# Optimization experiments

Measured on AMD Instinct MI355X. Metric: run time of the kernel, lower is better.

Reference implementation:

```python
import jax, jax.numpy as jnp
import numpy as np

KS, ST, SS, TOP_N, WIN = 32, 16, 64, 16, 512  # kernel_size, stride, select_size, top_n, window_size
NEG = -1e30


def setup_inputs() -> dict:
    key = jax.random.key(0)
    k0, k1, k2, k3 = jax.random.split(key, 4)
    B, S, H, Dqk, Dv = 1, 2048, 16, 128, 128
    q = jax.random.normal(k0, (B, S, H, Dqk), jnp.float32)
    k = jax.random.normal(k1, (B, S, H, Dqk), jnp.float32)
    v = jax.random.normal(k2, (B, S, H, Dv), jnp.float32)
    w_gate = jax.random.normal(k3, (Dqk, 3), jnp.float32) * (Dqk ** -0.5)
    b_gate = jnp.zeros((3,), jnp.float32)
    return {"q": q, "k": k, "v": v, "w_gate": w_gate, "b_gate": b_gate}


def _masked_probs(scores, mask):
    # numerically safe masked softmax; rows with no valid key yield all-zero probs
    s = jnp.where(mask, scores, NEG)
    lse = jax.nn.logsumexp(s, axis=-1, keepdims=True)
    return jnp.where(mask, jnp.exp(s - lse), 0.0)


def _nsa_forward(q, k, v, w_gate, b_gate):
    B, S, H, Dqk = q.shape
    scale = Dqk ** -0.5
    C = (S - KS) // ST + 1          # number of compressed blocks
    NSEL = S // SS                  # number of selection blocks
    tpos = jnp.arange(S)

    # ---- branch 1: compressed attention (mean-pooled K/V blocks) ----
    wpos = jnp.arange(C)[:, None] * ST + jnp.arange(KS)[None, :]   # [C,KS]
    cmp_k = k[:, wpos].mean(axis=2)                                # [B,C,H,Dqk]
    cmp_v = v[:, wpos].mean(axis=2)                                # [B,C,H,Dv]
    s_cmp = jnp.einsum('bqhd,bchd->bhqc', q, cmp_k) * scale
    cmp_end = jnp.arange(C) * ST + KS - 1
    cmask = cmp_end[None, :] <= tpos[:, None]                      # block fully in past
    p_cmp = _masked_probs(s_cmp, cmask)                            # [B,H,S,C]
    cmp_o = jnp.einsum('bhqc,bchd->bqhd', p_cmp, cmp_v)

    # ---- top-n block selection from compressed attention probs ----
    c_start = jnp.arange(C) * ST
    j_start = jnp.arange(NSEL) * SS
    overlap = ((c_start[:, None] < j_start[None, :] + SS) &
               (c_start[:, None] + KS > j_start[None, :])).astype(q.dtype)  # [C,NSEL]
    p_sel = jnp.einsum('bhqc,cj->bhqj', p_cmp, overlap)            # [B,H,S,NSEL]
    allowed = j_start[None, :] <= tpos[:, None]                    # block started
    cur_oh = jax.nn.one_hot(tpos // SS, NSEL, dtype=q.dtype)       # force current block
    sc = jnp.where(allowed, p_sel, -1.0) + 1e6 * cur_oh
    _, idx = jax.lax.top_k(sc, TOP_N)                              # [B,H,S,TOP_N]

    # ---- shared dense scores (reference only; real kernel is IO-aware) ----
    s_full = jnp.einsum('bqhd,bkhd->bhqk', q, k) * scale           # [B,H,S,S]
    causal = tpos[None, :] <= tpos[:, None]

    # ---- branch 2: selected-block attention ----
    blk_mask = (idx[..., None] == jnp.arange(NSEL)).any(axis=-2)   # [B,H,S,NSEL]
    key_blk = tpos // SS
    sel_mask = blk_mask[..., key_blk] & causal                     # [B,H,S,S]
    p_s = _masked_probs(s_full, sel_mask)
    select_o = jnp.einsum('bhqk,bkhd->bqhd', p_s, v)

    # ---- branch 3: sliding-window causal attention ----
    wmask = causal & ((tpos[:, None] - tpos[None, :]) <= WIN)
    p_w = _masked_probs(s_full, wmask)
    window_o = jnp.einsum('bhqk,bkhd->bqhd', p_w, v)

    # ---- learned per-query gates ----
    gate = jax.nn.sigmoid(jnp.einsum('bqhd,dg->bqhg', q, w_gate) + b_gate)
    return (cmp_o * gate[..., 0:1] + select_o * gate[..., 1:2]
            + window_o * gate[..., 2:3])


def reference(q, k, v, w_gate, b_gate):
    return _nsa_forward(q, k, v, w_gate, b_gate)
```

## Files before the change

### kernel.cpp

```cpp
#include <hip/hip_runtime.h>

#define S_LEN 2048
#define NH 16
#define DIM 128
#define KSZ 32
#define STRD 16
#define SSZ 64
#define NSELB 32
#define NCMP 127
#define TOPN 16
#define WINSZ 512
#define NEGF (-1e30f)
#define NEGTH (-1e29f)
#define SCALE 0.088388347648318447f

typedef __attribute__((ext_vector_type(8))) short bf16x8;
typedef __attribute__((ext_vector_type(4))) float f32x4;

__device__ __forceinline__ unsigned short f2bf(float f) {
  unsigned u = __builtin_bit_cast(unsigned, f);
  return (unsigned short)((u + 0x7FFFu + ((u >> 16) & 1u)) >> 16);
}
__device__ __forceinline__ bf16x8 pack8(const float* f) {
  bf16x8 r;
#pragma unroll
  for (int i = 0; i < 8; ++i) r[i] = (short)f2bf(f[i]);
  return r;
}

__global__ __launch_bounds__(256) void vt_build(const float* __restrict__ v,
                                                unsigned short* __restrict__ vtg) {
  const int c = blockIdx.x * 256 + threadIdx.x;
  const int h = c >> 15;
  const int rem = c & 32767;
  const int d = rem >> 8;
  const int tc = rem & 255;
  float f[8];
#pragma unroll
  for (int i = 0; i < 8; ++i) f[i] = v[((tc * 8 + i) * NH + h) * DIM + d];
  bf16x8 r = pack8(f);
  *(bf16x8*)(vtg + ((h * DIM + d) * S_LEN + tc * 8)) = r;
}

__global__ __launch_bounds__(128) void nsa_compress(
    const float* __restrict__ k, const float* __restrict__ v,
    unsigned short* __restrict__ cmpkb, unsigned short* __restrict__ cmpvt) {
  const int c = blockIdx.x & 127;
  const int h = blockIdx.x >> 7;
  const int d = threadIdx.x;
  float sk = 0.f, sv = 0.f;
  if (c < NCMP) {
    const int base = ((c * STRD) * NH + h) * DIM + d;
#pragma unroll
    for (int i = 0; i < KSZ; ++i) {
      sk += k[base + i * NH * DIM];
      sv += v[base + i * NH * DIM];
    }
    sk *= (1.0f / KSZ); sv *= (1.0f / KSZ);
  }
  cmpkb[(h * 128 + c) * 128 + d] = (c < NCMP) ? f2bf(sk) : 0;
  cmpvt[(h * 128 + d) * 128 + c] = (c < NCMP) ? f2bf(sv) : 0;
}

__global__ __launch_bounds__(256, 2) void nsa_main(
    const float* __restrict__ q, const float* __restrict__ k,
    const float* __restrict__ v, const float* __restrict__ wg,
    const float* __restrict__ bg, const unsigned short* __restrict__ vtg,
    const unsigned short* __restrict__ cmpkb, const unsigned short* __restrict__ cmpvt,
    float* __restrict__ out) {
  __shared__ __align__(16) char klds[32 * 256];
  __shared__ __align__(16) char vt[128 * 80];
  __shared__ __align__(16) float sc[4 * 16 * 132];
  __shared__ __align__(16) char pa[4 * 2048];
  __shared__ unsigned maskLds[64];
  __shared__ unsigned unionLds;
  __shared__ float gatesLds[192];

  const int h = blockIdx.x >> 5;
  const int t0 = (blockIdx.x & 31) * 64;
  const int tid = threadIdx.x;
  const int lane = tid & 63;
  const int w = tid >> 6;
  const int l15 = lane & 15;
  const int l4 = lane >> 4;

  float* scw = sc + w * 16 * 132;
  char* paw = pa + w * 2048;

  if (tid < 64) maskLds[tid] = 0u;
  if (tid == 64) unionLds = 0u;

  {
    const int qloc = tid >> 2, g = tid & 3;
    if (g < 3) {
      const int tq = t0 + qloc;
      const float* qr = q + (tq * NH + h) * DIM;
      float acc = bg[g];
#pragma unroll
      for (int d4 = 0; d4 < DIM; d4 += 4) {
        const float4 qv = *(const float4*)(qr + d4);
        acc += qv.x * wg[(d4 + 0) * 3 + g] + qv.y * wg[(d4 + 1) * 3 + g] +
               qv.z * wg[(d4 + 2) * 3 + g] + qv.w * wg[(d4 + 3) * 3 + g];
      }
      gatesLds[qloc * 3 + g] = 1.0f / (1.0f + __expf(-acc));
    }
  }

  bf16x8 qf[4];
  {
    const float* qp = q + ((t0 + w * 16 + l15) * NH + h) * DIM + l4 * 8;
#pragma unroll
    for (int ks = 0; ks < 4; ++ks) {
      float f[8];
#pragma unroll
      for (int i = 0; i < 4; ++i) f[i] = qp[ks * 32 + i];
#pragma unroll
      for (int i = 0; i < 4; ++i) f[4 + i] = qp[ks * 32 + 4 + i];
      qf[ks] = pack8(f);
    }
  }

  for (int ct = 0; ct < 4; ++ct) {
    __syncthreads();
#pragma unroll
    for (int c = 0; c < 2; ++c) {
      const int e = tid + c * 256;
      const int key = e >> 4, dc = e & 15;
      *(bf16x8*)(klds + key * 256 + ((dc * 16) ^ ((key & 7) << 4))) =
          *(const bf16x8*)(cmpkb + (h * 128 + ct * 32 + key) * 128 + dc * 8);
    }
    __syncthreads();
    f32x4 s0 = {0, 0, 0, 0}, s1 = {0, 0, 0, 0};
#pragma unroll
    for (int ks = 0; ks < 4; ++ks) {
      const int db = ks * 64 + l4 * 16;
      bf16x8 b0 = *(const bf16x8*)(klds + l15 * 256 + (db ^ ((l15 & 7) << 4)));
      bf16x8 b1 = *(const bf16x8*)(klds + (16 + l15) * 256 + (db ^ (((16 + l15) & 7) << 4)));
      s0 = __builtin_amdgcn_mfma_f32_16x16x32_bf16(qf[ks], b0, s0, 0, 0, 0);
      s1 = __builtin_amdgcn_mfma_f32_16x16x32_bf16(qf[ks], b1, s1, 0, 0, 0);
    }
#pragma unroll
    for (int j = 0; j < 4; ++j) {
      const int qr = l4 * 4 + j;
      scw[qr * 132 + ct * 32 + l15] = s0[j] * SCALE;
      scw[qr * 132 + ct * 32 + 16 + l15] = s1[j] * SCALE;
    }
  }
  __syncthreads();

  {
    const int qq = lane >> 2, qg = lane & 3;
    const int tq = t0 + w * 16 + qq;
    const int nv = (tq >= KSZ - 1) ? ((tq - (KSZ - 1)) / STRD + 1) : 0;
    float x[32];
#pragma unroll
    for (int i = 0; i < 32; ++i) x[i] = scw[qq * 132 + qg * 32 + i];
    float m = NEGF;
#pragma unroll
    for (int i = 0; i < 32; ++i) {
      const int c = qg * 32 + i;
      if (c < nv) m = fmaxf(m, x[i]);
    }
    m = fmaxf(m, __shfl_xor(m, 1));
    m = fmaxf(m, __shfl_xor(m, 2));
    float s = 0.f;
#pragma unroll
    for (int i = 0; i < 32; ++i) {
      const int c = qg * 32 + i;
      x[i] = (c < nv) ? __expf(x[i] - m) : 0.f;
      s += x[i];
    }
    s += __shfl_xor(s, 1);
    s += __shfl_xor(s, 2);
    const float inv = (nv > 0) ? (1.0f / s) : 0.f;
#pragma unroll
    for (int i = 0; i < 32; ++i) scw[qq * 132 + qg * 32 + i] = x[i] * inv;
  }
  __syncthreads();

  {
    const int qq = lane >> 2, jg = lane & 3;
    const int tq = t0 + w * 16 + qq;
    float* ss = (float*)paw;
    float vj[8];
#pragma unroll
    for (int i = 0; i < 8; ++i) {
      const int j = jg * 8 + i;
      const int lo = (4 * j - 1 > 0) ? 4 * j - 1 : 0;
      const int hi = (4 * j + 3 < NCMP - 1) ? 4 * j + 3 : NCMP - 1;
      float ps = 0.f;
      for (int c = lo; c <= hi; ++c) ps += scw[qq * 132 + c];
      float val = (j * SSZ <= tq) ? ps : -1.0f;
      if (j == (tq >> 6)) val += 1e6f;
      vj[i] = val;
      ss[qq * 32 + j] = val;
    }
    __syncthreads();
#pragma unroll
    for (int i = 0; i < 8; ++i) {
      const int j = jg * 8 + i;
      const float my = vj[i];
      int rank = 0;
      for (int jp = 0; jp < NSELB; ++jp) {
        const float o = ss[qq * 32 + jp];
        rank += (o > my) || (o == my && jp < j);
      }
      if (rank < TOPN && (j * SSZ <= tq)) {
        atomicOr(&maskLds[w * 16 + qq], 1u << j);
        atomicOr(&unionLds, 1u << j);
      }
    }
  }
  __syncthreads();

  unsigned maskq[4];
#pragma unroll
  for (int j = 0; j < 4; ++j) maskq[j] = maskLds[w * 16 + l4 * 4 + j];
  const unsigned unionMask = unionLds;

  f32x4 accA[8], accB[8];
#pragma unroll
  for (int n = 0; n < 8; ++n) accA[n] = (f32x4){0, 0, 0, 0};
  for (int ct = 0; ct < 4; ++ct) {
    __syncthreads();
#pragma unroll
    for (int c = 0; c < 2; ++c) {
      const int e = tid + c * 256;
      const int d = e >> 2, kc = e & 3;
      *(bf16x8*)(vt + d * 80 + kc * 16) =
          *(const bf16x8*)(cmpvt + (h * 128 + d) * 128 + ct * 32 + kc * 8);
    }
    __syncthreads();
    float f[8];
#pragma unroll
    for (int i = 0; i < 8; ++i) f[i] = scw[l15 * 132 + ct * 32 + l4 * 8 + i];
    bf16x8 ap = pack8(f);
#pragma unroll
    for (int n = 0; n < 8; ++n) {
      bf16x8 bv = *(const bf16x8*)(vt + (n * 16 + l15) * 80 + l4 * 16);
      accA[n] = __builtin_amdgcn_mfma_f32_16x16x32_bf16(ap, bv, accA[n], 0, 0, 0);
    }
  }
  __syncthreads();
#pragma unroll
  for (int j = 0; j < 4; ++j) {
    const int qr = l4 * 4 + j;
    const float g0 = gatesLds[(w * 16 + qr) * 3 + 0];
#pragma unroll
    for (int n = 0; n < 8; ++n) scw[qr * 132 + n * 16 + l15] = g0 * accA[n][j];
  }

  float mS[4], lS[4], mW[4], lW[4];
#pragma unroll
  for (int j = 0; j < 4; ++j) { mS[j] = NEGF; lS[j] = 0.f; mW[j] = NEGF; lW[j] = 0.f; }
#pragma unroll
  for (int n = 0; n < 8; ++n) { accA[n] = (f32x4){0, 0, 0, 0}; accB[n] = (f32x4){0, 0, 0, 0}; }

  const int ktmax = (t0 + 63) >> 5;
  for (int kt = 0; kt <= ktmax; ++kt) {
    const int kt0 = kt * 32;
    const int jb = kt >> 1;
    const bool selAny = (unionMask >> jb) & 1u;
    const bool winAny = (kt0 + 31) >= (t0 - WINSZ);
    if (!selAny && !winAny) continue;
    __syncthreads();
#pragma unroll
    for (int c = 0; c < 2; ++c) {
      const int e = tid + c * 256;
      const int key = e >> 4, dc = e & 15;
      const float* src = k + ((kt0 + key) * NH + h) * DIM + dc * 8;
      float f[8];
#pragma unroll
      for (int i = 0; i < 8; ++i) f[i] = src[i];
      *(bf16x8*)(klds + key * 256 + ((dc * 16) ^ ((key & 7) << 4))) = pack8(f);
    }
#pragma unroll
    for (int c = 0; c < 2; ++c) {
      const int e = tid + c * 256;
      const int d = e >> 2, kc = e & 3;
      *(bf16x8*)(vt + d * 80 + kc * 16) =
          *(const bf16x8*)(vtg + (h * 128 + d) * S_LEN + kt0 + kc * 8);
    }
    __syncthreads();

    f32x4 s0 = {0, 0, 0, 0}, s1 = {0, 0, 0, 0};
#pragma unroll
    for (int ks = 0; ks < 4; ++ks) {
      const int db = ks * 64 + l4 * 16;
      bf16x8 b0 = *(const bf16x8*)(klds + l15 * 256 + (db ^ ((l15 & 7) << 4)));
      bf16x8 b1 = *(const bf16x8*)(klds + (16 + l15) * 256 + (db ^ (((16 + l15) & 7) << 4)));
      s0 = __builtin_amdgcn_mfma_f32_16x16x32_bf16(qf[ks], b0, s0, 0, 0, 0);
      s1 = __builtin_amdgcn_mfma_f32_16x16x32_bf16(qf[ks], b1, s1, 0, 0, 0);
    }
#pragma unroll
    for (int j = 0; j < 4; ++j) { s0[j] *= SCALE; s1[j] *= SCALE; }
    const int c0 = kt0 + l15, c1 = kt0 + 16 + l15;

    if (selAny) {
#pragma unroll
      for (int j = 0; j < 4; ++j) {
        const int qr = l4 * 4 + j;
        const int tq = t0 + w * 16 + qr;
        const bool mb = (maskq[j] >> jb) & 1u;
        const float v0 = (mb && c0 <= tq) ? s0[j] : NEGF;
        const float v1 = (mb && c1 <= tq) ? s1[j] : NEGF;
        float rm = fmaxf(v0, v1);
        rm = fmaxf(rm, __shfl_xor(rm, 1));
        rm = fmaxf(rm, __shfl_xor(rm, 2));
        rm = fmaxf(rm, __shfl_xor(rm, 4));
        rm = fmaxf(rm, __shfl_xor(rm, 8));
        const float mn = fmaxf(mS[j], rm);
        const float sf = __expf(mS[j] - mn);
        const float p0 = (v0 > NEGTH) ? __expf(v0 - mn) : 0.f;
        const float p1 = (v1 > NEGTH) ? __expf(v1 - mn) : 0.f;
        float rs = p0 + p1;
        rs += __shfl_xor(rs, 1);
        rs += __shfl_xor(rs, 2);
        rs += __shfl_xor(rs, 4);
        rs += __shfl_xor(rs, 8);
        lS[j] = lS[j] * sf + rs;
        mS[j] = mn;
#pragma unroll
        for (int n = 0; n < 8; ++n) accA[n][j] *= sf;
        *(unsigned short*)(paw + qr * 128 + ((l15 * 2) ^ ((qr & 7) << 4))) = f2bf(p0);
        *(unsigned short*)(paw + qr * 128 + (((16 + l15) * 2) ^ ((qr & 7) << 4))) = f2bf(p1);
      }
      bf16x8 ap = *(const bf16x8*)(paw + l15 * 128 + ((l4 * 16) ^ ((l15 & 7) << 4)));
#pragma unroll
      for (int n = 0; n < 8; ++n) {
        bf16x8 bv = *(const bf16x8*)(vt + (n * 16 + l15) * 80 + l4 * 16);
        accA[n] = __builtin_amdgcn_mfma_f32_16x16x32_bf16(ap, bv, accA[n], 0, 0, 0);
      }
    }
    if (winAny) {
#pragma unroll
      for (int j = 0; j < 4; ++j) {
        const int qr = l4 * 4 + j;
        const int tq = t0 + w * 16 + qr;
        const float v0 = (c0 <= tq && c0 >= tq - WINSZ) ? s0[j] : NEGF;
        const float v1 = (c1 <= tq && c1 >= tq - WINSZ) ? s1[j] : NEGF;
        float rm = fmaxf(v0, v1);
        rm = fmaxf(rm, __shfl_xor(rm, 1));
        rm = fmaxf(rm, __shfl_xor(rm, 2));
        rm = fmaxf(rm, __shfl_xor(rm, 4));
        rm = fmaxf(rm, __shfl_xor(rm, 8));
        const float mn = fmaxf(mW[j], rm);
        const float sf = __expf(mW[j] - mn);
        const float p0 = (v0 > NEGTH) ? __expf(v0 - mn) : 0.f;
        const float p1 = (v1 > NEGTH) ? __expf(v1 - mn) : 0.f;
        float rs = p0 + p1;
        rs += __shfl_xor(rs, 1);
        rs += __shfl_xor(rs, 2);
        rs += __shfl_xor(rs, 4);
        rs += __shfl_xor(rs, 8);
        lW[j] = lW[j] * sf + rs;
        mW[j] = mn;
#pragma unroll
        for (int n = 0; n < 8; ++n) accB[n][j] *= sf;
        *(unsigned short*)(paw + qr * 128 + ((l15 * 2) ^ ((qr & 7) << 4))) = f2bf(p0);
        *(unsigned short*)(paw + qr * 128 + (((16 + l15) * 2) ^ ((qr & 7) << 4))) = f2bf(p1);
      }
      bf16x8 ap = *(const bf16x8*)(paw + l15 * 128 + ((l4 * 16) ^ ((l15 & 7) << 4)));
#pragma unroll
      for (int n = 0; n < 8; ++n) {
        bf16x8 bv = *(const bf16x8*)(vt + (n * 16 + l15) * 80 + l4 * 16);
        accB[n] = __builtin_amdgcn_mfma_f32_16x16x32_bf16(ap, bv, accB[n], 0, 0, 0);
      }
    }
  }

#pragma unroll
  for (int j = 0; j < 4; ++j) {
    const int qr = l4 * 4 + j;
    const int tq = t0 + w * 16 + qr;
    const float g1 = gatesLds[(w * 16 + qr) * 3 + 1];
    const float g2 = gatesLds[(w * 16 + qr) * 3 + 2];
    const float rlS = 1.0f / lS[j];
    const float rlW = 1.0f / lW[j];
#pragma unroll
    for (int n = 0; n < 8; ++n) {
      const float val = scw[qr * 132 + n * 16 + l15] + g1 * accA[n][j] * rlS +
                        g2 * accB[n][j] * rlW;
      out[(tq * NH + h) * DIM + n * 16 + l15] = val;
    }
  }
}

extern "C" void kernel_launch(void* const* d_in, const int* in_sizes, int n_in,
                              void* d_out, int out_size, void* d_ws, size_t ws_size,
                              hipStream_t stream) {
  const float* q  = (const float*)d_in[0];
  const float* k  = (const float*)d_in[1];
  const float* v  = (const float*)d_in[2];
  const float* wg = (const float*)d_in[3];
  const float* bg = (const float*)d_in[4];
  float* out = (float*)d_out;

  unsigned short* vtg   = (unsigned short*)d_ws;
  unsigned short* cmpkb = vtg + NH * DIM * S_LEN;
  unsigned short* cmpvt = cmpkb + NH * 128 * 128;

  vt_build<<<2048, 256, 0, stream>>>(v, vtg);
  nsa_compress<<<NH * 128, 128, 0, stream>>>(k, v, cmpkb, cmpvt);
  nsa_main<<<NH * 32, 256, 0, stream>>>(q, k, v, wg, bg, vtg, cmpkb, cmpvt, out);
}
```

Measured before the change: 242.0 us.

## Split compressed QK into bf16 hi/lo terms and pre-convert K to bf16

Computes the compressed-attention scores with a three-term bf16 split (hi*hi + lo*hi + hi*lo), so top-k block selection is closer to fp32 precision. K is converted to bf16 once in a pre-pass, which removes the per-block fp32 load and convert inside the main loop. The online softmax now rescales only when the running max rises. The gated compressed output is kept in registers instead of LDS, which drops one barrier. The split adds MFMA work and LDS loads in the compressed stage, plus extra registers and workspace.

```diff
diff --git a/kernel.cpp b/kernel.cpp
--- a/kernel.cpp
+++ b/kernel.cpp
@@ -21,6 +21,9 @@
   unsigned u = __builtin_bit_cast(unsigned, f);
   return (unsigned short)((u + 0x7FFFu + ((u >> 16) & 1u)) >> 16);
 }
+__device__ __forceinline__ float bf2f(unsigned short b) {
+  return __builtin_bit_cast(float, (unsigned)b << 16);
+}
 __device__ __forceinline__ bf16x8 pack8(const float* f) {
   bf16x8 r;
 #pragma unroll
@@ -28,23 +31,32 @@
   return r;
 }
 
-__global__ __launch_bounds__(256) void vt_build(const float* __restrict__ v,
-                                                unsigned short* __restrict__ vtg) {
+__global__ __launch_bounds__(256) void nsa_build(
+    const float* __restrict__ v, const float* __restrict__ k,
+    unsigned short* __restrict__ vtg, unsigned short* __restrict__ kb) {
   const int c = blockIdx.x * 256 + threadIdx.x;
-  const int h = c >> 15;
-  const int rem = c & 32767;
-  const int d = rem >> 8;
-  const int tc = rem & 255;
-  float f[8];
-#pragma unroll
-  for (int i = 0; i < 8; ++i) f[i] = v[((tc * 8 + i) * NH + h) * DIM + d];
-  bf16x8 r = pack8(f);
-  *(bf16x8*)(vtg + ((h * DIM + d) * S_LEN + tc * 8)) = r;
+  {
+    const int h = c >> 15, rem = c & 32767;
+    const int d = rem >> 8, tc = rem & 255;
+    float f[8];
+#pragma unroll
+    for (int i = 0; i < 8; ++i) f[i] = v[((tc * 8 + i) * NH + h) * DIM + d];
+    *(bf16x8*)(vtg + ((h * DIM + d) * S_LEN + tc * 8)) = pack8(f);
+  }
+  {
+    const int t = c >> 8, h2 = (c >> 4) & 15, dc = c & 15;
+    const float* src = k + ((t * NH + h2) * DIM + dc * 8);
+    float f[8];
+#pragma unroll
+    for (int i = 0; i < 8; ++i) f[i] = src[i];
+    *(bf16x8*)(kb + (t * NH + h2) * DIM + dc * 8) = pack8(f);
+  }
 }
 
 __global__ __launch_bounds__(128) void nsa_compress(
     const float* __restrict__ k, const float* __restrict__ v,
-    unsigned short* __restrict__ cmpkb, unsigned short* __restrict__ cmpvt) {
+    unsigned short* __restrict__ cmpkh, unsigned short* __restrict__ cmpkl,
+    unsigned short* __restrict__ cmpvt) {
   const int c = blockIdx.x & 127;
   const int h = blockIdx.x >> 7;
   const int d = threadIdx.x;
@@ -58,16 +70,19 @@
     }
     sk *= (1.0f / KSZ); sv *= (1.0f / KSZ);
   }
-  cmpkb[(h * 128 + c) * 128 + d] = (c < NCMP) ? f2bf(sk) : 0;
+  const unsigned short hi = f2bf(sk);
+  const unsigned short lo = f2bf(sk - bf2f(hi));
+  cmpkh[(h * 128 + c) * 128 + d] = (c < NCMP) ? hi : 0;
+  cmpkl[(h * 128 + c) * 128 + d] = (c < NCMP) ? lo : 0;
   cmpvt[(h * 128 + d) * 128 + c] = (c < NCMP) ? f2bf(sv) : 0;
 }
 
 __global__ __launch_bounds__(256, 2) void nsa_main(
-    const float* __restrict__ q, const float* __restrict__ k,
-    const float* __restrict__ v, const float* __restrict__ wg,
-    const float* __restrict__ bg, const unsigned short* __restrict__ vtg,
-    const unsigned short* __restrict__ cmpkb, const unsigned short* __restrict__ cmpvt,
-    float* __restrict__ out) {
+    const float* __restrict__ q, const float* __restrict__ wg,
+    const float* __restrict__ bg, const unsigned short* __restrict__ kb,
+    const unsigned short* __restrict__ vtg,
+    const unsigned short* __restrict__ cmpkh, const unsigned short* __restrict__ cmpkl,
+    const unsigned short* __restrict__ cmpvt, float* __restrict__ out) {
   __shared__ __align__(16) char klds[32 * 256];
   __shared__ __align__(16) char vt[128 * 80];
   __shared__ __align__(16) float sc[4 * 16 * 132];
@@ -86,6 +101,7 @@
 
   float* scw = sc + w * 16 * 132;
   char* paw = pa + w * 2048;
+  char* kldsL = vt;
 
   if (tid < 64) maskLds[tid] = 0u;
   if (tid == 64) unionLds = 0u;
@@ -93,8 +109,7 @@
   {
     const int qloc = tid >> 2, g = tid & 3;
     if (g < 3) {
-      const int tq = t0 + qloc;
-      const float* qr = q + (tq * NH + h) * DIM;
+      const float* qr = q + ((t0 + qloc) * NH + h) * DIM;
       float acc = bg[g];
 #pragma unroll
       for (int d4 = 0; d4 < DIM; d4 += 4) {
@@ -106,17 +121,21 @@
     }
   }
 
-  bf16x8 qf[4];
+  bf16x8 qfh[4], qfl[4];
   {
     const float* qp = q + ((t0 + w * 16 + l15) * NH + h) * DIM + l4 * 8;
 #pragma unroll
     for (int ks = 0; ks < 4; ++ks) {
-      float f[8];
-#pragma unroll
-      for (int i = 0; i < 4; ++i) f[i] = qp[ks * 32 + i];
-#pragma unroll
-      for (int i = 0; i < 4; ++i) f[4 + i] = qp[ks * 32 + 4 + i];
-      qf[ks] = pack8(f);
+      float fh[8], fl[8];
+#pragma unroll
+      for (int i = 0; i < 8; ++i) {
+        const float x = qp[ks * 32 + i];
+        const unsigned short hb = f2bf(x);
+        fh[i] = bf2f(hb);
+        fl[i] = x - fh[i];
+      }
+      qfh[ks] = pack8(fh);
+      qfl[ks] = pack8(fl);
     }
   }
 
@@ -126,18 +145,28 @@
     for (int c = 0; c < 2; ++c) {
       const int e = tid + c * 256;
       const int key = e >> 4, dc = e & 15;
-      *(bf16x8*)(klds + key * 256 + ((dc * 16) ^ ((key & 7) << 4))) =
-          *(const bf16x8*)(cmpkb + (h * 128 + ct * 32 + key) * 128 + dc * 8);
+      const int swz = key * 256 + ((dc * 16) ^ ((key & 7) << 4));
+      const int src = (h * 128 + ct * 32 + key) * 128 + dc * 8;
+      *(bf16x8*)(klds + swz) = *(const bf16x8*)(cmpkh + src);
+      *(bf16x8*)(kldsL + swz) = *(const bf16x8*)(cmpkl + src);
     }
     __syncthreads();
     f32x4 s0 = {0, 0, 0, 0}, s1 = {0, 0, 0, 0};
 #pragma unroll
     for (int ks = 0; ks < 4; ++ks) {
       const int db = ks * 64 + l4 * 16;
-      bf16x8 b0 = *(const bf16x8*)(klds + l15 * 256 + (db ^ ((l15 & 7) << 4)));
-      bf16x8 b1 = *(const bf16x8*)(klds + (16 + l15) * 256 + (db ^ (((16 + l15) & 7) << 4)));
-      s0 = __builtin_amdgcn_mfma_f32_16x16x32_bf16(qf[ks], b0, s0, 0, 0, 0);
-      s1 = __builtin_amdgcn_mfma_f32_16x16x32_bf16(qf[ks], b1, s1, 0, 0, 0);
+      const int o0 = l15 * 256 + (db ^ ((l15 & 7) << 4));
+      const int o1 = (16 + l15) * 256 + (db ^ (((16 + l15) & 7) << 4));
+      bf16x8 bh0 = *(const bf16x8*)(klds + o0);
+      bf16x8 bh1 = *(const bf16x8*)(klds + o1);
+      bf16x8 bl0 = *(const bf16x8*)(kldsL + o0);
+      bf16x8 bl1 = *(const bf16x8*)(kldsL + o1);
+      s0 = __builtin_amdgcn_mfma_f32_16x16x32_bf16(qfh[ks], bh0, s0, 0, 0, 0);
+      s0 = __builtin_amdgcn_mfma_f32_16x16x32_bf16(qfl[ks], bh0, s0, 0, 0, 0);
+      s0 = __builtin_amdgcn_mfma_f32_16x16x32_bf16(qfh[ks], bl0, s0, 0, 0, 0);
+      s1 = __builtin_amdgcn_mfma_f32_16x16x32_bf16(qfh[ks], bh1, s1, 0, 0, 0);
+      s1 = __builtin_amdgcn_mfma_f32_16x16x32_bf16(qfl[ks], bh1, s1, 0, 0, 0);
+      s1 = __builtin_amdgcn_mfma_f32_16x16x32_bf16(qfh[ks], bl1, s1, 0, 0, 0);
     }
 #pragma unroll
     for (int j = 0; j < 4; ++j) {
@@ -218,7 +247,7 @@
   for (int j = 0; j < 4; ++j) maskq[j] = maskLds[w * 16 + l4 * 4 + j];
   const unsigned unionMask = unionLds;
 
-  f32x4 accA[8], accB[8];
+  f32x4 accA[8], accB[8], ocmp[8];
 #pragma unroll
   for (int n = 0; n < 8; ++n) accA[n] = (f32x4){0, 0, 0, 0};
   for (int ct = 0; ct < 4; ++ct) {
@@ -241,13 +270,11 @@
       accA[n] = __builtin_amdgcn_mfma_f32_16x16x32_bf16(ap, bv, accA[n], 0, 0, 0);
     }
   }
-  __syncthreads();
 #pragma unroll
   for (int j = 0; j < 4; ++j) {
-    const int qr = l4 * 4 + j;
-    const float g0 = gatesLds[(w * 16 + qr) * 3 + 0];
-#pragma unroll
-    for (int n = 0; n < 8; ++n) scw[qr * 132 + n * 16 + l15] = g0 * accA[n][j];
+    const float g0 = gatesLds[(w * 16 + l4 * 4 + j) * 3 + 0];
+#pragma unroll
+    for (int n = 0; n < 8; ++n) ocmp[n][j] = g0 * accA[n][j];
   }
 
   float mS[4], lS[4], mW[4], lW[4];
@@ -268,18 +295,15 @@
     for (int c = 0; c < 2; ++c) {
       const int e = tid + c * 256;
       const int key = e >> 4, dc = e & 15;
-      const float* src = k + ((kt0 + key) * NH + h) * DIM + dc * 8;
-      float f[8];
-#pragma unroll
-      for (int i = 0; i < 8; ++i) f[i] = src[i];
-      *(bf16x8*)(klds + key * 256 + ((dc * 16) ^ ((key & 7) << 4))) = pack8(f);
+      *(bf16x8*)(klds + key * 256 + ((dc * 16) ^ ((key & 7) << 4))) =
+          *(const bf16x8*)(kb + ((kt0 + key) * NH + h) * DIM + dc * 8);
     }
 #pragma unroll
     for (int c = 0; c < 2; ++c) {
       const int e = tid + c * 256;
       const int d = e >> 2, kc = e & 3;
       *(bf16x8*)(vt + d * 80 + kc * 16) =
-          *(const bf16x8*)(vtg + (h * 128 + d) * S_LEN + kt0 + kc * 8);
+          *(const bf16x8*)(vtg + (h * DIM + d) * S_LEN + kt0 + kc * 8);
     }
     __syncthreads();
 
@@ -289,8 +313,8 @@
       const int db = ks * 64 + l4 * 16;
       bf16x8 b0 = *(const bf16x8*)(klds + l15 * 256 + (db ^ ((l15 & 7) << 4)));
       bf16x8 b1 = *(const bf16x8*)(klds + (16 + l15) * 256 + (db ^ (((16 + l15) & 7) << 4)));
-      s0 = __builtin_amdgcn_mfma_f32_16x16x32_bf16(qf[ks], b0, s0, 0, 0, 0);
-      s1 = __builtin_amdgcn_mfma_f32_16x16x32_bf16(qf[ks], b1, s1, 0, 0, 0);
+      s0 = __builtin_amdgcn_mfma_f32_16x16x32_bf16(qfh[ks], b0, s0, 0, 0, 0);
+      s1 = __builtin_amdgcn_mfma_f32_16x16x32_bf16(qfh[ks], b1, s1, 0, 0, 0);
     }
 #pragma unroll
     for (int j = 0; j < 4; ++j) { s0[j] *= SCALE; s1[j] *= SCALE; }
@@ -309,19 +333,21 @@
         rm = fmaxf(rm, __shfl_xor(rm, 2));
         rm = fmaxf(rm, __shfl_xor(rm, 4));
         rm = fmaxf(rm, __shfl_xor(rm, 8));
-        const float mn = fmaxf(mS[j], rm);
-        const float sf = __expf(mS[j] - mn);
-        const float p0 = (v0 > NEGTH) ? __expf(v0 - mn) : 0.f;
-        const float p1 = (v1 > NEGTH) ? __expf(v1 - mn) : 0.f;
+        if (rm > mS[j]) {
+          const float sf = __expf(mS[j] - rm);
+          lS[j] *= sf;
+#pragma unroll
+          for (int n = 0; n < 8; ++n) accA[n][j] *= sf;
+          mS[j] = rm;
+        }
+        const float p0 = (v0 > NEGTH) ? __expf(v0 - mS[j]) : 0.f;
+        const float p1 = (v1 > NEGTH) ? __expf(v1 - mS[j]) : 0.f;
         float rs = p0 + p1;
         rs += __shfl_xor(rs, 1);
         rs += __shfl_xor(rs, 2);
         rs += __shfl_xor(rs, 4);
         rs += __shfl_xor(rs, 8);
-        lS[j] = lS[j] * sf + rs;
-        mS[j] = mn;
-#pragma unroll
-        for (int n = 0; n < 8; ++n) accA[n][j] *= sf;
+        lS[j] += rs;
         *(unsigned short*)(paw + qr * 128 + ((l15 * 2) ^ ((qr & 7) << 4))) = f2bf(p0);
         *(unsigned short*)(paw + qr * 128 + (((16 + l15) * 2) ^ ((qr & 7) << 4))) = f2bf(p1);
       }
@@ -344,19 +370,21 @@
         rm = fmaxf(rm, __shfl_xor(rm, 2));
         rm = fmaxf(rm, __shfl_xor(rm, 4));
         rm = fmaxf(rm, __shfl_xor(rm, 8));
-        const float mn = fmaxf(mW[j], rm);
-        const float sf = __expf(mW[j] - mn);
-        const float p0 = (v0 > NEGTH) ? __expf(v0 - mn) : 0.f;
-        const float p1 = (v1 > NEGTH) ? __expf(v1 - mn) : 0.f;
+        if (rm > mW[j]) {
+          const float sf = __expf(mW[j] - rm);
+          lW[j] *= sf;
+#pragma unroll
+          for (int n = 0; n < 8; ++n) accB[n][j] *= sf;
+          mW[j] = rm;
+        }
+        const float p0 = (v0 > NEGTH) ? __expf(v0 - mW[j]) : 0.f;
+        const float p1 = (v1 > NEGTH) ? __expf(v1 - mW[j]) : 0.f;
         float rs = p0 + p1;
         rs += __shfl_xor(rs, 1);
         rs += __shfl_xor(rs, 2);
         rs += __shfl_xor(rs, 4);
         rs += __shfl_xor(rs, 8);
-        lW[j] = lW[j] * sf + rs;
-        mW[j] = mn;
-#pragma unroll
-        for (int n = 0; n < 8; ++n) accB[n][j] *= sf;
+        lW[j] += rs;
         *(unsigned short*)(paw + qr * 128 + ((l15 * 2) ^ ((qr & 7) << 4))) = f2bf(p0);
         *(unsigned short*)(paw + qr * 128 + (((16 + l15) * 2) ^ ((qr & 7) << 4))) = f2bf(p1);
       }
@@ -379,9 +407,8 @@
     const float rlW = 1.0f / lW[j];
 #pragma unroll
     for (int n = 0; n < 8; ++n) {
-      const float val = scw[qr * 132 + n * 16 + l15] + g1 * accA[n][j] * rlS +
-                        g2 * accB[n][j] * rlW;
-      out[(tq * NH + h) * DIM + n * 16 + l15] = val;
+      out[(tq * NH + h) * DIM + n * 16 + l15] =
+          ocmp[n][j] + g1 * accA[n][j] * rlS + g2 * accB[n][j] * rlW;
     }
   }
 }
@@ -397,10 +424,12 @@
   float* out = (float*)d_out;
 
   unsigned short* vtg   = (unsigned short*)d_ws;
-  unsigned short* cmpkb = vtg + NH * DIM * S_LEN;
-  unsigned short* cmpvt = cmpkb + NH * 128 * 128;
-
-  vt_build<<<2048, 256, 0, stream>>>(v, vtg);
-  nsa_compress<<<NH * 128, 128, 0, stream>>>(k, v, cmpkb, cmpvt);
-  nsa_main<<<NH * 32, 256, 0, stream>>>(q, k, v, wg, bg, vtg, cmpkb, cmpvt, out);
-}
+  unsigned short* kb    = vtg + NH * DIM * S_LEN;
+  unsigned short* cmpkh = kb + S_LEN * NH * DIM;
+  unsigned short* cmpkl = cmpkh + NH * 128 * 128;
+  unsigned short* cmpvt = cmpkl + NH * 128 * 128;
+
+  nsa_build<<<2048, 256, 0, stream>>>(v, k, vtg, kb);
+  nsa_compress<<<NH * 128, 128, 0, stream>>>(k, v, cmpkh, cmpkl, cmpvt);
+  nsa_main<<<NH * 32, 256, 0, stream>>>(q, wg, bg, kb, vtg, cmpkh, cmpkl, cmpvt, out);
+}
```

Measured after the change: 263.7 us. +9.0%, slower.
